# Kernel tuning notes

Measured on AMD Instinct MI355X. Metric: run time of the kernel, lower is better.

Reference implementation:

```python
import jax, jax.numpy as jnp
import numpy as np

B, L, H, E = 2, 2048, 8, 64
S = L  # self-attention


def setup_inputs() -> dict:
    key = jax.random.key(0)
    k1, k2, k3, k4, k5 = jax.random.split(key, 5)
    return {
        "queries": jax.random.normal(k1, (B, L, H, E), dtype=jnp.float32),
        "keys": jax.random.normal(k2, (B, S, H, E), dtype=jnp.float32),
        "values": jax.random.normal(k3, (B, S, H, E), dtype=jnp.float32),
        "tau": jax.random.uniform(k4, (B, 1), dtype=jnp.float32),
        "delta": jax.random.normal(k5, (B, S), dtype=jnp.float32),
    }


def reference(queries, keys, values, tau, delta):
    # De-stationary attention: scores = (QK^T) * tau + delta, causal mask, softmax, AV
    E_ = queries.shape[-1]
    scale = 1.0 / jnp.sqrt(jnp.float32(E_))
    tau_b = tau[:, None, None, :]      # [B,1,1,1]
    delta_b = delta[:, None, None, :]  # [B,1,1,S]
    scores = jnp.einsum('blhe,bshe->bhls', queries, keys) * tau_b + delta_b  # [B,H,L,S]
    Lq, Sk = scores.shape[-2], scores.shape[-1]
    causal = jnp.triu(jnp.ones((Lq, Sk), dtype=bool), k=1)  # True = masked
    scores = jnp.where(causal[None, None], -jnp.inf, scores)
    A = jax.nn.softmax(scale * scores, axis=-1)
    V = jnp.einsum('bhls,bshd->blhd', A, values)
    return V
```

## Files before the change

kernel.cpp:

```cpp
#include <hip/hip_runtime.h>


typedef _Float16 h8 __attribute__((ext_vector_type(8)));
typedef _Float16 h2 __attribute__((ext_vector_type(2)));
typedef float f32x4 __attribute__((ext_vector_type(4)));

constexpr int Bc = 2, Lc = 2048, Hc = 8, Ec = 64, Sc = 2048;
constexpr int QTL = 128;
constexpr int NQT = Lc / QTL;
constexpr int KT = 64;
constexpr int LDK = 72;
constexpr int NBH = Bc * Hc;
constexpr float SCALE = 0.125f;
constexpr float LOG2E = 1.44269504088896340736f;

__device__ __forceinline__ h2 pk2(float x, float y) {
  return __builtin_bit_cast(h2, __builtin_amdgcn_cvt_pkrtz(x, y));
}
template <int CTRL>
__device__ __forceinline__ float dpp_f(float x) {
  int r = __builtin_amdgcn_update_dpp(0, __builtin_bit_cast(int, x), CTRL, 0xF, 0xF, true);
  return __builtin_bit_cast(float, r);
}

template <int CH_IT, int EPB, int NIT>
__global__ __launch_bounds__(256, 2)
void dsattn_fwd(const float* __restrict__ Qg, const float* __restrict__ Kg,
                const float* __restrict__ Vg, const float* __restrict__ taug,
                const float* __restrict__ deltag, float* __restrict__ Og,
                _Float16* __restrict__ Opart, float* __restrict__ Lpart) {
  __shared__ __align__(16) _Float16 Ks[2][KT * LDK];
  __shared__ __align__(16) _Float16 Vt[2][Ec * LDK];
  __shared__ __align__(16) _Float16 Pb[4][16 * LDK];

  const int tid = threadIdx.x;
  const int wave = tid >> 6, lane = tid & 63;
  const int quad = lane >> 4, l16 = lane & 15;
  const int srow = tid >> 2;
  const int sec = (tid & 3) << 4;
  const int vrp = ((tid >> 3) + 4 * (tid & 7)) & 31;
  const int ve8 = (tid & 7) << 3;
  _Float16* pb = &Pb[wave][0];
  const int lo = l16 & 1;
  const int pbase = (lo ? 32 : 0) + (l16 & ~1);

  h8 onesf;
#pragma unroll
  for (int j = 0; j < 8; ++j) onesf[j] = (_Float16)1.0f;

  for (int wid = (int)blockIdx.x; wid < NIT; wid += (int)gridDim.x) {
    const int bh = wid & (NBH - 1);
    const int e = wid >> 4;
    int qt = NQT - 1, c0 = 0, pre_e = 0;
    {
      int ee = e, acc = 0;
#pragma unroll
      for (int q = NQT - 1; q >= 0; --q) {
        const int n = (2 * q + 1 + CH_IT) / CH_IT;
        if (ee < n) { qt = q; c0 = ee; pre_e = EPB - acc - n; break; }
        ee -= n; acc += n;
      }
    }
    const int ntiles = 2 * qt + 2;
    const int nch = (ntiles + CH_IT - 1) / CH_IT;
    const int ktBeg = c0 * CH_IT;
    const int ktEnd = min(ktBeg + CH_IT - 1, ntiles - 1);
    const int q0 = qt * QTL;
    const int b = bh >> 3, h = bh & 7;
    const float ct = taug[b] * (SCALE * LOG2E);

    h8 qfrag[2][2];
#pragma unroll
    for (int f = 0; f < 2; ++f)
#pragma unroll
      for (int kk = 0; kk < 2; ++kk) {
        const float* qp = Qg + (((size_t)b * Lc + q0 + 32 * wave + 16 * f + l16) * Hc + h) * Ec
                         + quad * 8 + kk * 32;
        const float4* p = (const float4*)qp;
        union { h8 v; h2 c[4]; } u;
        float4 a0 = p[0], a1 = p[1];
        u.c[0] = pk2(a0.x, a0.y); u.c[1] = pk2(a0.z, a0.w);
        u.c[2] = pk2(a1.x, a1.y); u.c[3] = pk2(a1.z, a1.w);
        qfrag[f][kk] = u.v;
      }

    f32x4 Oacc[2][4], Osum[2];
#pragma unroll
    for (int f = 0; f < 2; ++f) {
#pragma unroll
      for (int nt = 0; nt < 4; ++nt) Oacc[f][nt] = (f32x4){0.f, 0.f, 0.f, 0.f};
      Osum[f] = (f32x4){0.f, 0.f, 0.f, 0.f};
    }

    float dcur[4];

    __syncthreads();

    {
      const int kb = ktBeg * KT;
      const float* kp = Kg + (((size_t)b * Sc + kb + srow) * Hc + h) * Ec + sec;
      float4 c0v = ((const float4*)kp)[0], c1v = ((const float4*)kp)[1];
      float4 c2v = ((const float4*)kp)[2], c3v = ((const float4*)kp)[3];
      const float* vp0 = Vg + (((size_t)b * Sc + kb + 2 * vrp) * Hc + h) * Ec + ve8;
      const float* vp1 = vp0 + Hc * Ec;
      float4 r00 = ((const float4*)vp0)[0], r01 = ((const float4*)vp0)[1];
      float4 r10 = ((const float4*)vp1)[0], r11 = ((const float4*)vp1)[1];
#pragma unroll
      for (int nt = 0; nt < 4; ++nt)
        dcur[nt] = deltag[(size_t)b * Sc + kb + nt * 16 + l16] * (SCALE * LOG2E);
      union { h8 v; h2 c[4]; } w0, w1;
      w0.c[0] = pk2(c0v.x, c0v.y); w0.c[1] = pk2(c0v.z, c0v.w);
      w0.c[2] = pk2(c1v.x, c1v.y); w0.c[3] = pk2(c1v.z, c1v.w);
      w1.c[0] = pk2(c2v.x, c2v.y); w1.c[1] = pk2(c2v.z, c2v.w);
      w1.c[2] = pk2(c3v.x, c3v.y); w1.c[3] = pk2(c3v.z, c3v.w);
      *(h8*)&Ks[0][srow * LDK + sec] = w0.v;
      *(h8*)&Ks[0][srow * LDK + sec + 8] = w1.v;
      const float e0[8] = {r00.x, r00.y, r00.z, r00.w, r01.x, r01.y, r01.z, r01.w};
      const float e1[8] = {r10.x, r10.y, r10.z, r10.w, r11.x, r11.y, r11.z, r11.w};
#pragma unroll
      for (int j = 0; j < 8; ++j)
        *(h2*)&Vt[0][(ve8 + j) * LDK + 2 * vrp] = pk2(e0[j], e1[j]);
    }

    for (int kt = ktBeg; kt <= ktEnd; ++kt) {
      const int cur = (kt - ktBeg) & 1;
      const bool pf = (kt < ktEnd);
      const int kbase = kt * KT;

      __syncthreads();

      float4 kn0, kn1, kn2, kn3, vn00, vn01, vn10, vn11;
      float dn[4];
      if (pf) {
        const int nb = (kt + 1) * KT;
        const float* kp = Kg + (((size_t)b * Sc + nb + srow) * Hc + h) * Ec + sec;
        kn0 = ((const float4*)kp)[0]; kn1 = ((const float4*)kp)[1];
        kn2 = ((const float4*)kp)[2]; kn3 = ((const float4*)kp)[3];
        const float* vp0 = Vg + (((size_t)b * Sc + nb + 2 * vrp) * Hc + h) * Ec + ve8;
        const float* vp1 = vp0 + Hc * Ec;
        vn00 = ((const float4*)vp0)[0]; vn01 = ((const float4*)vp0)[1];
        vn10 = ((const float4*)vp1)[0]; vn11 = ((const float4*)vp1)[1];
#pragma unroll
        for (int nt = 0; nt < 4; ++nt)
          dn[nt] = deltag[(size_t)b * Sc + nb + nt * 16 + l16];
      }

      const int wtop = q0 + 32 * wave + 31;
      if (kbase <= wtop) {
        f32x4 Sacc[2][4];
#pragma unroll
        for (int f = 0; f < 2; ++f)
#pragma unroll
          for (int nt = 0; nt < 4; ++nt) Sacc[f][nt] = (f32x4){0.f, 0.f, 0.f, 0.f};
#pragma unroll
        for (int kk = 0; kk < 2; ++kk) {
          h8 bf[4];
#pragma unroll
          for (int nt = 0; nt < 4; ++nt)
            bf[nt] = *(const h8*)&Ks[cur][(nt * 16 + l16) * LDK + quad * 8 + kk * 32];
#pragma unroll
          for (int f = 0; f < 2; ++f)
#pragma unroll
            for (int nt = 0; nt < 4; ++nt)
              Sacc[f][nt] = __builtin_amdgcn_mfma_f32_16x16x32_f16(qfrag[f][kk], bf[nt], Sacc[f][nt], 0, 0, 0);
        }

#pragma unroll
        for (int f = 0; f < 2; ++f) {
          const int fr0 = q0 + 32 * wave + 16 * f;
          float sv[4][4];
#pragma unroll
          for (int nt = 0; nt < 4; ++nt)
#pragma unroll
            for (int r = 0; r < 4; ++r)
              sv[nt][r] = Sacc[f][nt][r] * ct + dcur[nt];
          if (kbase + 63 > fr0) {
#pragma unroll
            for (int nt = 0; nt < 4; ++nt) {
              const int key = kbase + nt * 16 + l16;
#pragma unroll
              for (int r = 0; r < 4; ++r)
                if (key > fr0 + quad * 4 + r) sv[nt][r] = -1e30f;
            }
          }
#pragma unroll
          for (int nt = 0; nt < 4; ++nt)
#pragma unroll
            for (int r = 0; r < 4; ++r)
              sv[nt][r] = __builtin_amdgcn_exp2f(sv[nt][r]);

#pragma unroll
          for (int r = 0; r < 4; ++r) {
            float o0 = dpp_f<0xB1>(sv[0][r]);
            float o1 = dpp_f<0xB1>(sv[1][r]);
            float o2 = dpp_f<0xB1>(sv[2][r]);
            float o3 = dpp_f<0xB1>(sv[3][r]);
            h2 d0 = lo ? pk2(o2, sv[2][r]) : pk2(sv[0][r], o0);
            h2 d1 = lo ? pk2(o3, sv[3][r]) : pk2(sv[1][r], o1);
            _Float16* pp = &pb[((quad << 2) + r) * LDK + pbase];
            *(h2*)pp = d0;
            *(h2*)(pp + 16) = d1;
          }
          asm volatile("s_waitcnt lgkmcnt(0)" ::: "memory");

          h8 af0 = *(const h8*)&pb[l16 * LDK + quad * 8];
          h8 af1 = *(const h8*)&pb[l16 * LDK + quad * 8 + 32];

#pragma unroll
          for (int nt = 0; nt < 4; ++nt) {
            h8 vf0 = *(const h8*)&Vt[cur][(nt * 16 + l16) * LDK + quad * 8];
            Oacc[f][nt] = __builtin_amdgcn_mfma_f32_16x16x32_f16(af0, vf0, Oacc[f][nt], 0, 0, 0);
            h8 vf1 = *(const h8*)&Vt[cur][(nt * 16 + l16) * LDK + quad * 8 + 32];
            Oacc[f][nt] = __builtin_amdgcn_mfma_f32_16x16x32_f16(af1, vf1, Oacc[f][nt], 0, 0, 0);
          }
          Osum[f] = __builtin_amdgcn_mfma_f32_16x16x32_f16(af0, onesf, Osum[f], 0, 0, 0);
          Osum[f] = __builtin_amdgcn_mfma_f32_16x16x32_f16(af1, onesf, Osum[f], 0, 0, 0);
        }
      }

      if (pf) {
        _Float16* ksn = &Ks[cur ^ 1][0];
        _Float16* vtn = &Vt[cur ^ 1][0];
        union { h8 v; h2 c[4]; } w0, w1;
        w0.c[0] = pk2(kn0.x, kn0.y); w0.c[1] = pk2(kn0.z, kn0.w);
        w0.c[2] = pk2(kn1.x, kn1.y); w0.c[3] = pk2(kn1.z, kn1.w);
        w1.c[0] = pk2(kn2.x, kn2.y); w1.c[1] = pk2(kn2.z, kn2.w);
        w1.c[2] = pk2(kn3.x, kn3.y); w1.c[3] = pk2(kn3.z, kn3.w);
        *(h8*)&ksn[srow * LDK + sec] = w0.v;
        *(h8*)&ksn[srow * LDK + sec + 8] = w1.v;
        const float e0[8] = {vn00.x, vn00.y, vn00.z, vn00.w, vn01.x, vn01.y, vn01.z, vn01.w};
        const float e1[8] = {vn10.x, vn10.y, vn10.z, vn10.w, vn11.x, vn11.y, vn11.z, vn11.w};
#pragma unroll
        for (int j = 0; j < 8; ++j)
          *(h2*)&vtn[(ve8 + j) * LDK + 2 * vrp] = pk2(e0[j], e1[j]);
#pragma unroll
        for (int nt = 0; nt < 4; ++nt) dcur[nt] = dn[nt] * (SCALE * LOG2E);
      }
    }

    if (nch == 1) {
#pragma unroll
      for (int f = 0; f < 2; ++f)
#pragma unroll
        for (int r = 0; r < 4; ++r) {
          const int qrow = q0 + 32 * wave + 16 * f + (quad << 2) + r;
          const float inv = 1.0f / Osum[f][r];
          float* op = Og + (((size_t)b * Lc + qrow) * Hc + h) * Ec;
#pragma unroll
          for (int nt = 0; nt < 4; ++nt) op[nt * 16 + l16] = Oacc[f][nt][r] * inv;
        }
    } else {
      const int en = bh * EPB + pre_e + c0;
      _Float16* op = Opart + (size_t)en * (QTL * Ec);
#pragma unroll
      for (int f = 0; f < 2; ++f)
#pragma unroll
        for (int r = 0; r < 4; ++r) {
          const int row = 32 * wave + 16 * f + (quad << 2) + r;
#pragma unroll
          for (int nt = 0; nt < 4; ++nt)
            op[row * Ec + nt * 16 + l16] = (_Float16)Oacc[f][nt][r];
          if (l16 == 0) Lpart[en * QTL + row] = Osum[f][r];
        }
    }
  }
}

template <int CH_IT, int EPB>
__global__ __launch_bounds__(256, 4)
void dsattn_comb(const _Float16* __restrict__ Opart, const float* __restrict__ Lpart,
                 float* __restrict__ Og) {
  const int qt = (CH_IT / 2) + ((int)blockIdx.x >> 2);
  const int slab = (int)blockIdx.x & 3;
  const int bh = (int)blockIdx.y;
  const int b = bh >> 3, h = bh & 7;
  const int nch = (2 * qt + 1 + CH_IT) / CH_IT;
  int pre_e = 0;
#pragma unroll
  for (int q = 0; q < NQT; ++q)
    if (q < qt) pre_e += (2 * q + 1 + CH_IT) / CH_IT;
  const int e0 = bh * EPB + pre_e;

  const int row = slab * 32 + ((int)threadIdx.x >> 3);
  const int col = ((int)threadIdx.x & 7) << 3;

  float acc[8];
#pragma unroll
  for (int i = 0; i < 8; ++i) acc[i] = 0.f;
  float l = 0.f;
  for (int c = 0; c < nch; ++c) {
    l += Lpart[(e0 + c) * QTL + row];
    h8 v = *(const h8*)(Opart + (size_t)(e0 + c) * (QTL * Ec) + row * Ec + col);
#pragma unroll
    for (int i = 0; i < 8; ++i) acc[i] += (float)v[i];
  }
  const float inv = 1.0f / l;
  float* out = Og + (((size_t)b * Lc + qt * QTL + row) * Hc + h) * Ec + col;
  float4 o0, o1;
  o0.x = acc[0] * inv; o0.y = acc[1] * inv; o0.z = acc[2] * inv; o0.w = acc[3] * inv;
  o1.x = acc[4] * inv; o1.y = acc[5] * inv; o1.z = acc[6] * inv; o1.w = acc[7] * inv;
  ((float4*)out)[0] = o0;
  ((float4*)out)[1] = o1;
}

extern "C" void kernel_launch(void* const* d_in, const int* in_sizes, int n_in,
                              void* d_out, int out_size, void* d_ws, size_t ws_size,
                              hipStream_t stream) {
  const float* Q = (const float*)d_in[0];
  const float* K = (const float*)d_in[1];
  const float* V = (const float*)d_in[2];
  const float* tau = (const float*)d_in[3];
  const float* delta = (const float*)d_in[4];
  float* O = (float*)d_out;

  constexpr int CH = 4;
  constexpr int EPB = 72;
  constexpr int TOT_E = Bc * Hc * EPB;
  constexpr int PERS = 768;
  const size_t need = (size_t)TOT_E * QTL * Ec * 2 + (size_t)TOT_E * QTL * 4;

  if (ws_size >= need) {
    _Float16* Opart = (_Float16*)d_ws;
    float* Lpart = (float*)(Opart + (size_t)TOT_E * QTL * Ec);
    dsattn_fwd<CH, EPB, TOT_E><<<dim3(PERS), 256, 0, stream>>>(
        Q, K, V, tau, delta, O, Opart, Lpart);
    dim3 g2((NQT - CH / 2) * 4, Bc * Hc);
    dsattn_comb<CH, EPB><<<g2, 256, 0, stream>>>(Opart, Lpart, O);
  } else {
    dsattn_fwd<32, NQT, NQT * NBH><<<dim3(NQT * NBH), 256, 0, stream>>>(
        Q, K, V, tau, delta, O, nullptr, nullptr);
  }
}
```

Measured before the change: 109.9 us.

## Pre-convert K/V to swizzled fp16 and stream tiles with global_load_lds

```diff
diff --git a/kernel.cpp b/kernel.cpp
--- a/kernel.cpp
+++ b/kernel.cpp
@@ -9,10 +9,48 @@
 constexpr int QTL = 128;
 constexpr int NQT = Lc / QTL;
 constexpr int KT = 64;
-constexpr int LDK = 72;
 constexpr int NBH = Bc * Hc;
+constexpr int CH = 4;
+constexpr int EPB = 72;
+constexpr int NIT = NBH * EPB;
 constexpr float SCALE = 0.125f;
 constexpr float LOG2E = 1.44269504088896340736f;
+
+__constant__ int d_qtbase[16] = {0,1,2,4,6,9,12,16,20,25,30,36,42,49,56,64};
+__constant__ signed char d_eqt[72] = {
+  15,15,15,15,15,15,15,15,
+  14,14,14,14,14,14,14,
+  13,13,13,13,13,13,13,
+  12,12,12,12,12,12,
+  11,11,11,11,11,11,
+  10,10,10,10,10,
+   9, 9, 9, 9, 9,
+   8, 8, 8, 8,
+   7, 7, 7, 7,
+   6, 6, 6,
+   5, 5, 5,
+   4, 4,
+   3, 3,
+   2,
+   1,
+  14,12,10, 8, 6, 4, 2, 0};
+__constant__ signed char d_ec0[72] = {
+   0, 1, 2, 3, 4, 5, 6, 7,
+   0, 1, 2, 3, 4, 5, 6,
+   0, 1, 2, 3, 4, 5, 6,
+   0, 1, 2, 3, 4, 5,
+   0, 1, 2, 3, 4, 5,
+   0, 1, 2, 3, 4,
+   0, 1, 2, 3, 4,
+   0, 1, 2, 3,
+   0, 1, 2, 3,
+   0, 1, 2,
+   0, 1, 2,
+   0, 1,
+   0, 1,
+   0,
+   0,
+   7, 6, 5, 4, 3, 2, 1, 0};
 
 __device__ __forceinline__ h2 pk2(float x, float y) {
   return __builtin_bit_cast(h2, __builtin_amdgcn_cvt_pkrtz(x, y));
@@ -22,18 +60,321 @@
   int r = __builtin_amdgcn_update_dpp(0, __builtin_bit_cast(int, x), CTRL, 0xF, 0xF, true);
   return __builtin_bit_cast(float, r);
 }
-
-template <int CH_IT, int EPB, int NIT>
+__device__ __forceinline__ void gl16(const void* g, void* l) {
+  __builtin_amdgcn_global_load_lds(
+      (const __attribute__((address_space(1))) void*)g,
+      (__attribute__((address_space(3))) void*)l, 16, 0, 0);
+}
+
+__global__ __launch_bounds__(256, 4)
+void dsattn_prep(const float* __restrict__ Kg, const float* __restrict__ Vg,
+                 _Float16* __restrict__ Kh, _Float16* __restrict__ Vh) {
+  __shared__ __align__(16) _Float16 T[64][72];
+  const int kt = (int)blockIdx.x;
+  const int bh = (int)blockIdx.y;
+  const int b = bh >> 3, h = bh & 7;
+  const int tid = (int)threadIdx.x;
+  const int sr = tid >> 2;
+  const int e0 = (tid & 3) << 4;
+  const int s = kt * KT + sr;
+
+  {
+    const float* kp = Kg + (((size_t)b * Sc + s) * Hc + h) * Ec + e0;
+    float4 a0 = ((const float4*)kp)[0], a1 = ((const float4*)kp)[1];
+    float4 a2 = ((const float4*)kp)[2], a3 = ((const float4*)kp)[3];
+    union { h8 v; h2 c[4]; } u0, u1;
+    u0.c[0] = pk2(a0.x, a0.y); u0.c[1] = pk2(a0.z, a0.w);
+    u0.c[2] = pk2(a1.x, a1.y); u0.c[3] = pk2(a1.z, a1.w);
+    u1.c[0] = pk2(a2.x, a2.y); u1.c[1] = pk2(a2.z, a2.w);
+    u1.c[2] = pk2(a3.x, a3.y); u1.c[3] = pk2(a3.z, a3.w);
+    char* out = (char*)Kh + (((size_t)bh * Sc + s) << 7);
+    const int sl = e0 >> 3;
+    const int rx = (sr & 7) << 4;
+    *(h8*)(out + ((sl << 4) ^ rx)) = u0.v;
+    *(h8*)(out + (((sl + 1) << 4) ^ rx)) = u1.v;
+  }
+
+  {
+    const float* vp = Vg + (((size_t)b * Sc + s) * Hc + h) * Ec + e0;
+    float4 v0 = ((const float4*)vp)[0], v1 = ((const float4*)vp)[1];
+    float4 v2 = ((const float4*)vp)[2], v3 = ((const float4*)vp)[3];
+    const float ev[16] = {v0.x, v0.y, v0.z, v0.w, v1.x, v1.y, v1.z, v1.w,
+                          v2.x, v2.y, v2.z, v2.w, v3.x, v3.y, v3.z, v3.w};
+#pragma unroll
+    for (int j = 0; j < 8; ++j) {
+      h2 t = pk2(ev[2 * j], ev[2 * j + 1]);
+      T[e0 + 2 * j][sr] = t[0];
+      T[e0 + 2 * j + 1][sr] = t[1];
+    }
+  }
+  __syncthreads();
+  {
+    const int er = tid >> 2;
+    const int k0 = (tid & 3) << 4;
+    h8 w0 = *(const h8*)&T[er][k0];
+    h8 w1 = *(const h8*)&T[er][k0 + 8];
+    char* out = (char*)Vh + (((size_t)bh * 32 + kt) << 13) + er * 128;
+    const int sl = k0 >> 3;
+    const int rx = (er & 7) << 4;
+    *(h8*)(out + ((sl << 4) ^ rx)) = w0;
+    *(h8*)(out + (((sl + 1) << 4) ^ rx)) = w1;
+  }
+}
+
+__global__ __launch_bounds__(256, 4)
+void dsattn_fwd_main(const float* __restrict__ Qg, const _Float16* __restrict__ Kh,
+                     const _Float16* __restrict__ Vh, const float* __restrict__ taug,
+                     const float* __restrict__ deltag, float* __restrict__ Og,
+                     _Float16* __restrict__ Opart, float* __restrict__ Lpart) {
+  __shared__ __align__(16) _Float16 Ks[2][KT * 64];
+  __shared__ __align__(16) _Float16 Vt[2][Ec * 64];
+  __shared__ __align__(16) _Float16 Pb[4][16 * 64];
+
+  const int tid = (int)threadIdx.x;
+  const int wave = tid >> 6, lane = tid & 63;
+  const int quad = lane >> 4, l16 = lane & 15;
+  _Float16* pb = &Pb[wave][0];
+  const int lo = l16 & 1;
+  const int pbase = (lo ? 32 : 0) + (l16 & ~1);
+  const int kx = (l16 & 7) << 3;
+  const int koff0 = (quad * 8) ^ kx;
+  const int koff1 = (quad * 8 + 32) ^ kx;
+
+  h8 onesf;
+#pragma unroll
+  for (int j = 0; j < 8; ++j) onesf[j] = (_Float16)1.0f;
+
+  for (int it = (int)blockIdx.x; it < NIT; it += (int)gridDim.x) {
+    const int xcd = it & 7;
+    const int r_ = it >> 3;
+    const int bh = (xcd << 1) | (r_ & 1);
+    const int e = r_ >> 1;
+    const int qt = d_eqt[e], c0 = d_ec0[e];
+    const int ntiles = 2 * qt + 2;
+    const int nch = (ntiles + CH - 1) / CH;
+    const int ktBeg = c0 * CH;
+    const int ktEnd = min(ktBeg + CH - 1, ntiles - 1);
+    const int q0 = qt * QTL;
+    const int b = bh >> 3, h = bh & 7;
+    const float ct = taug[b] * (SCALE * LOG2E);
+
+    h8 qfrag[2][2];
+#pragma unroll
+    for (int f = 0; f < 2; ++f)
+#pragma unroll
+      for (int kk = 0; kk < 2; ++kk) {
+        const float* qp = Qg + (((size_t)b * Lc + q0 + 32 * wave + 16 * f + l16) * Hc + h) * Ec
+                         + quad * 8 + kk * 32;
+        const float4* p = (const float4*)qp;
+        union { h8 v; h2 c[4]; } u;
+        float4 a0 = p[0], a1 = p[1];
+        u.c[0] = pk2(a0.x, a0.y); u.c[1] = pk2(a0.z, a0.w);
+        u.c[2] = pk2(a1.x, a1.y); u.c[3] = pk2(a1.z, a1.w);
+        qfrag[f][kk] = u.v;
+      }
+
+    f32x4 Oacc[2][4], Osum[2];
+#pragma unroll
+    for (int f = 0; f < 2; ++f) {
+#pragma unroll
+      for (int nt = 0; nt < 4; ++nt) Oacc[f][nt] = (f32x4){0.f, 0.f, 0.f, 0.f};
+      Osum[f] = (f32x4){0.f, 0.f, 0.f, 0.f};
+    }
+    float dcur[4];
+
+    __syncthreads();
+
+    {
+      const char* kg = (const char*)Kh + (((size_t)bh * Sc + (size_t)ktBeg * KT) << 7)
+                       + wave * 2048 + lane * 16;
+      const char* vg = (const char*)Vh + (((size_t)bh * 32 + ktBeg) << 13)
+                       + wave * 2048 + lane * 16;
+      char* kl = (char*)&Ks[0][0] + wave * 2048;
+      char* vl = (char*)&Vt[0][0] + wave * 2048;
+      gl16(kg, kl); gl16(kg + 1024, kl + 1024);
+      gl16(vg, vl); gl16(vg + 1024, vl + 1024);
+#pragma unroll
+      for (int nt = 0; nt < 4; ++nt)
+        dcur[nt] = deltag[(size_t)b * Sc + ktBeg * KT + nt * 16 + l16] * (SCALE * LOG2E);
+    }
+
+    for (int kt = ktBeg; kt <= ktEnd; ++kt) {
+      const int cur = (kt - ktBeg) & 1;
+      const bool pf = (kt < ktEnd);
+      const int kbase = kt * KT;
+
+      __syncthreads();
+
+      float dn[4];
+      if (pf) {
+        const char* kg = (const char*)Kh + (((size_t)bh * Sc + (size_t)(kt + 1) * KT) << 7)
+                         + wave * 2048 + lane * 16;
+        const char* vg = (const char*)Vh + (((size_t)bh * 32 + kt + 1) << 13)
+                         + wave * 2048 + lane * 16;
+        char* kl = (char*)&Ks[cur ^ 1][0] + wave * 2048;
+        char* vl = (char*)&Vt[cur ^ 1][0] + wave * 2048;
+        gl16(kg, kl); gl16(kg + 1024, kl + 1024);
+        gl16(vg, vl); gl16(vg + 1024, vl + 1024);
+#pragma unroll
+        for (int nt = 0; nt < 4; ++nt)
+          dn[nt] = deltag[(size_t)b * Sc + (kt + 1) * KT + nt * 16 + l16];
+      }
+
+      const int wtop = q0 + 32 * wave + 31;
+      if (kbase <= wtop) {
+        f32x4 Sacc[2][4];
+#pragma unroll
+        for (int f = 0; f < 2; ++f)
+#pragma unroll
+          for (int nt = 0; nt < 4; ++nt) Sacc[f][nt] = (f32x4){0.f, 0.f, 0.f, 0.f};
+        __builtin_amdgcn_s_setprio(1);
+#pragma unroll
+        for (int kk = 0; kk < 2; ++kk) {
+          const int ko = kk ? koff1 : koff0;
+          h8 bf[4];
+#pragma unroll
+          for (int nt = 0; nt < 4; ++nt)
+            bf[nt] = *(const h8*)&Ks[cur][(nt * 16 + l16) * 64 + ko];
+#pragma unroll
+          for (int f = 0; f < 2; ++f)
+#pragma unroll
+            for (int nt = 0; nt < 4; ++nt)
+              Sacc[f][nt] = __builtin_amdgcn_mfma_f32_16x16x32_f16(qfrag[f][kk], bf[nt], Sacc[f][nt], 0, 0, 0);
+        }
+        __builtin_amdgcn_s_setprio(0);
+
+#pragma unroll
+        for (int f = 0; f < 2; ++f) {
+          const int fr0 = q0 + 32 * wave + 16 * f;
+          float sv[4][4];
+#pragma unroll
+          for (int nt = 0; nt < 4; ++nt)
+#pragma unroll
+            for (int rr = 0; rr < 4; ++rr)
+              sv[nt][rr] = Sacc[f][nt][rr] * ct + dcur[nt];
+          if (kbase + 63 > fr0) {
+#pragma unroll
+            for (int nt = 0; nt < 4; ++nt) {
+              const int key = kbase + nt * 16 + l16;
+#pragma unroll
+              for (int rr = 0; rr < 4; ++rr)
+                if (key > fr0 + quad * 4 + rr) sv[nt][rr] = -1e30f;
+            }
+          }
+#pragma unroll
+          for (int nt = 0; nt < 4; ++nt)
+#pragma unroll
+            for (int rr = 0; rr < 4; ++rr)
+              sv[nt][rr] = __builtin_amdgcn_exp2f(sv[nt][rr]);
+
+#pragma unroll
+          for (int rr = 0; rr < 4; ++rr) {
+            float o0 = dpp_f<0xB1>(sv[0][rr]);
+            float o1 = dpp_f<0xB1>(sv[1][rr]);
+            float o2 = dpp_f<0xB1>(sv[2][rr]);
+            float o3 = dpp_f<0xB1>(sv[3][rr]);
+            h2 d0 = lo ? pk2(o2, sv[2][rr]) : pk2(sv[0][rr], o0);
+            h2 d1 = lo ? pk2(o3, sv[3][rr]) : pk2(sv[1][rr], o1);
+            const int row = (quad << 2) + rr;
+            char* pr = (char*)pb + row * 128;
+            const int rx = (row & 7) << 4;
+            *(h2*)(pr + ((pbase * 2) ^ rx)) = d0;
+            *(h2*)(pr + ((pbase * 2 + 32) ^ rx)) = d1;
+          }
+          asm volatile("s_waitcnt lgkmcnt(0)" ::: "memory");
+
+          h8 af0 = *(const h8*)&pb[l16 * 64 + koff0];
+          h8 af1 = *(const h8*)&pb[l16 * 64 + koff1];
+
+          __builtin_amdgcn_s_setprio(1);
+#pragma unroll
+          for (int nt = 0; nt < 4; ++nt) {
+            h8 vf0 = *(const h8*)&Vt[cur][(nt * 16 + l16) * 64 + koff0];
+            Oacc[f][nt] = __builtin_amdgcn_mfma_f32_16x16x32_f16(af0, vf0, Oacc[f][nt], 0, 0, 0);
+            h8 vf1 = *(const h8*)&Vt[cur][(nt * 16 + l16) * 64 + koff1];
+            Oacc[f][nt] = __builtin_amdgcn_mfma_f32_16x16x32_f16(af1, vf1, Oacc[f][nt], 0, 0, 0);
+          }
+          Osum[f] = __builtin_amdgcn_mfma_f32_16x16x32_f16(af0, onesf, Osum[f], 0, 0, 0);
+          Osum[f] = __builtin_amdgcn_mfma_f32_16x16x32_f16(af1, onesf, Osum[f], 0, 0, 0);
+          __builtin_amdgcn_s_setprio(0);
+        }
+      }
+
+      if (pf) {
+#pragma unroll
+        for (int nt = 0; nt < 4; ++nt) dcur[nt] = dn[nt] * (SCALE * LOG2E);
+      }
+    }
+
+    if (nch == 1) {
+#pragma unroll
+      for (int f = 0; f < 2; ++f)
+#pragma unroll
+        for (int rr = 0; rr < 4; ++rr) {
+          const int qrow = q0 + 32 * wave + 16 * f + (quad << 2) + rr;
+          const float inv = 1.0f / Osum[f][rr];
+          float* op = Og + (((size_t)b * Lc + qrow) * Hc + h) * Ec;
+#pragma unroll
+          for (int nt = 0; nt < 4; ++nt) op[nt * 16 + l16] = Oacc[f][nt][rr] * inv;
+        }
+    } else {
+      const int en = bh * EPB + d_qtbase[qt] + c0;
+      _Float16* op = Opart + (size_t)en * (QTL * Ec);
+#pragma unroll
+      for (int f = 0; f < 2; ++f)
+#pragma unroll
+        for (int rr = 0; rr < 4; ++rr) {
+          const int row = 32 * wave + 16 * f + (quad << 2) + rr;
+#pragma unroll
+          for (int nt = 0; nt < 4; ++nt)
+            op[row * Ec + nt * 16 + l16] = (_Float16)Oacc[f][nt][rr];
+          if (l16 == 0) Lpart[en * QTL + row] = Osum[f][rr];
+        }
+    }
+  }
+}
+
+__global__ __launch_bounds__(256, 4)
+void dsattn_comb_main(const _Float16* __restrict__ Opart, const float* __restrict__ Lpart,
+                      float* __restrict__ Og) {
+  const int qt = 2 + ((int)blockIdx.x >> 2);
+  const int slab = (int)blockIdx.x & 3;
+  const int bh = (int)blockIdx.y;
+  const int b = bh >> 3, h = bh & 7;
+  const int nch = (2 * qt + 1 + CH) / CH;
+  const int e0 = bh * EPB + d_qtbase[qt];
+  const int row = slab * 32 + ((int)threadIdx.x >> 3);
+  const int col = ((int)threadIdx.x & 7) << 3;
+
+  float acc[8];
+#pragma unroll
+  for (int i = 0; i < 8; ++i) acc[i] = 0.f;
+  float l = 0.f;
+  for (int c = 0; c < nch; ++c) {
+    l += Lpart[(e0 + c) * QTL + row];
+    h8 v = *(const h8*)(Opart + (size_t)(e0 + c) * (QTL * Ec) + row * Ec + col);
+#pragma unroll
+    for (int i = 0; i < 8; ++i) acc[i] += (float)v[i];
+  }
+  const float inv = 1.0f / l;
+  float* out = Og + (((size_t)b * Lc + qt * QTL + row) * Hc + h) * Ec + col;
+  float4 o0, o1;
+  o0.x = acc[0] * inv; o0.y = acc[1] * inv; o0.z = acc[2] * inv; o0.w = acc[3] * inv;
+  o1.x = acc[4] * inv; o1.y = acc[5] * inv; o1.z = acc[6] * inv; o1.w = acc[7] * inv;
+  ((float4*)out)[0] = o0;
+  ((float4*)out)[1] = o1;
+}
+
 __global__ __launch_bounds__(256, 2)
-void dsattn_fwd(const float* __restrict__ Qg, const float* __restrict__ Kg,
-                const float* __restrict__ Vg, const float* __restrict__ taug,
-                const float* __restrict__ deltag, float* __restrict__ Og,
-                _Float16* __restrict__ Opart, float* __restrict__ Lpart) {
+void dsattn_fwd_mono(const float* __restrict__ Qg, const float* __restrict__ Kg,
+                     const float* __restrict__ Vg, const float* __restrict__ taug,
+                     const float* __restrict__ deltag, float* __restrict__ Og) {
+  constexpr int LDK = 72;
   __shared__ __align__(16) _Float16 Ks[2][KT * LDK];
   __shared__ __align__(16) _Float16 Vt[2][Ec * LDK];
   __shared__ __align__(16) _Float16 Pb[4][16 * LDK];
 
-  const int tid = threadIdx.x;
+  const int tid = (int)threadIdx.x;
   const int wave = tid >> 6, lane = tid & 63;
   const int quad = lane >> 4, l16 = lane & 15;
   const int srow = tid >> 2;
@@ -48,23 +389,10 @@
 #pragma unroll
   for (int j = 0; j < 8; ++j) onesf[j] = (_Float16)1.0f;
 
-  for (int wid = (int)blockIdx.x; wid < NIT; wid += (int)gridDim.x) {
+  for (int wid = (int)blockIdx.x; wid < NQT * NBH; wid += (int)gridDim.x) {
     const int bh = wid & (NBH - 1);
-    const int e = wid >> 4;
-    int qt = NQT - 1, c0 = 0, pre_e = 0;
-    {
-      int ee = e, acc = 0;
-#pragma unroll
-      for (int q = NQT - 1; q >= 0; --q) {
-        const int n = (2 * q + 1 + CH_IT) / CH_IT;
-        if (ee < n) { qt = q; c0 = ee; pre_e = EPB - acc - n; break; }
-        ee -= n; acc += n;
-      }
-    }
-    const int ntiles = 2 * qt + 2;
-    const int nch = (ntiles + CH_IT - 1) / CH_IT;
-    const int ktBeg = c0 * CH_IT;
-    const int ktEnd = min(ktBeg + CH_IT - 1, ntiles - 1);
+    const int qt = NQT - 1 - (wid >> 4);
+    const int ktEnd = 2 * qt + 1;
     const int q0 = qt * QTL;
     const int b = bh >> 3, h = bh & 7;
     const float ct = taug[b] * (SCALE * LOG2E);
@@ -91,23 +419,21 @@
       for (int nt = 0; nt < 4; ++nt) Oacc[f][nt] = (f32x4){0.f, 0.f, 0.f, 0.f};
       Osum[f] = (f32x4){0.f, 0.f, 0.f, 0.f};
     }
-
     float dcur[4];
 
     __syncthreads();
 
     {
-      const int kb = ktBeg * KT;
-      const float* kp = Kg + (((size_t)b * Sc + kb + srow) * Hc + h) * Ec + sec;
+      const float* kp = Kg + (((size_t)b * Sc + srow) * Hc + h) * Ec + sec;
       float4 c0v = ((const float4*)kp)[0], c1v = ((const float4*)kp)[1];
       float4 c2v = ((const float4*)kp)[2], c3v = ((const float4*)kp)[3];
-      const float* vp0 = Vg + (((size_t)b * Sc + kb + 2 * vrp) * Hc + h) * Ec + ve8;
+      const float* vp0 = Vg + (((size_t)b * Sc + 2 * vrp) * Hc + h) * Ec + ve8;
       const float* vp1 = vp0 + Hc * Ec;
       float4 r00 = ((const float4*)vp0)[0], r01 = ((const float4*)vp0)[1];
       float4 r10 = ((const float4*)vp1)[0], r11 = ((const float4*)vp1)[1];
 #pragma unroll
       for (int nt = 0; nt < 4; ++nt)
-        dcur[nt] = deltag[(size_t)b * Sc + kb + nt * 16 + l16] * (SCALE * LOG2E);
+        dcur[nt] = deltag[(size_t)b * Sc + nt * 16 + l16] * (SCALE * LOG2E);
       union { h8 v; h2 c[4]; } w0, w1;
       w0.c[0] = pk2(c0v.x, c0v.y); w0.c[1] = pk2(c0v.z, c0v.w);
       w0.c[2] = pk2(c1v.x, c1v.y); w0.c[3] = pk2(c1v.z, c1v.w);
@@ -122,8 +448,8 @@
         *(h2*)&Vt[0][(ve8 + j) * LDK + 2 * vrp] = pk2(e0[j], e1[j]);
     }
 
-    for (int kt = ktBeg; kt <= ktEnd; ++kt) {
-      const int cur = (kt - ktBeg) & 1;
+    for (int kt = 0; kt <= ktEnd; ++kt) {
+      const int cur = kt & 1;
       const bool pf = (kt < ktEnd);
       const int kbase = kt * KT;
 
@@ -172,32 +498,32 @@
 #pragma unroll
           for (int nt = 0; nt < 4; ++nt)
 #pragma unroll
-            for (int r = 0; r < 4; ++r)
-              sv[nt][r] = Sacc[f][nt][r] * ct + dcur[nt];
+            for (int rr = 0; rr < 4; ++rr)
+              sv[nt][rr] = Sacc[f][nt][rr] * ct + dcur[nt];
           if (kbase + 63 > fr0) {
 #pragma unroll
             for (int nt = 0; nt < 4; ++nt) {
               const int key = kbase + nt * 16 + l16;
 #pragma unroll
-              for (int r = 0; r < 4; ++r)
-                if (key > fr0 + quad * 4 + r) sv[nt][r] = -1e30f;
+              for (int rr = 0; rr < 4; ++rr)
+                if (key > fr0 + quad * 4 + rr) sv[nt][rr] = -1e30f;
             }
           }
 #pragma unroll
           for (int nt = 0; nt < 4; ++nt)
 #pragma unroll
-            for (int r = 0; r < 4; ++r)
-              sv[nt][r] = __builtin_amdgcn_exp2f(sv[nt][r]);
-
-#pragma unroll
-          for (int r = 0; r < 4; ++r) {
-            float o0 = dpp_f<0xB1>(sv[0][r]);
-            float o1 = dpp_f<0xB1>(sv[1][r]);
-            float o2 = dpp_f<0xB1>(sv[2][r]);
-            float o3 = dpp_f<0xB1>(sv[3][r]);
-            h2 d0 = lo ? pk2(o2, sv[2][r]) : pk2(sv[0][r], o0);
-            h2 d1 = lo ? pk2(o3, sv[3][r]) : pk2(sv[1][r], o1);
-            _Float16* pp = &pb[((quad << 2) + r) * LDK + pbase];
+            for (int rr = 0; rr < 4; ++rr)
+              sv[nt][rr] = __builtin_amdgcn_exp2f(sv[nt][rr]);
+
+#pragma unroll
+          for (int rr = 0; rr < 4; ++rr) {
+            float o0 = dpp_f<0xB1>(sv[0][rr]);
+            float o1 = dpp_f<0xB1>(sv[1][rr]);
+            float o2 = dpp_f<0xB1>(sv[2][rr]);
+            float o3 = dpp_f<0xB1>(sv[3][rr]);
+            h2 d0 = lo ? pk2(o2, sv[2][rr]) : pk2(sv[0][rr], o0);
+            h2 d1 = lo ? pk2(o3, sv[3][rr]) : pk2(sv[1][rr], o1);
+            _Float16* pp = &pb[((quad << 2) + rr) * LDK + pbase];
             *(h2*)pp = d0;
             *(h2*)(pp + 16) = d1;
           }
@@ -238,69 +564,17 @@
       }
     }
 
-    if (nch == 1) {
-#pragma unroll
-      for (int f = 0; f < 2; ++f)
-#pragma unroll
-        for (int r = 0; r < 4; ++r) {
-          const int qrow = q0 + 32 * wave + 16 * f + (quad << 2) + r;
-          const float inv = 1.0f / Osum[f][r];
-          float* op = Og + (((size_t)b * Lc + qrow) * Hc + h) * Ec;
-#pragma unroll
-          for (int nt = 0; nt < 4; ++nt) op[nt * 16 + l16] = Oacc[f][nt][r] * inv;
-        }
-    } else {
-      const int en = bh * EPB + pre_e + c0;
-      _Float16* op = Opart + (size_t)en * (QTL * Ec);
-#pragma unroll
-      for (int f = 0; f < 2; ++f)
-#pragma unroll
-        for (int r = 0; r < 4; ++r) {
-          const int row = 32 * wave + 16 * f + (quad << 2) + r;
-#pragma unroll
-          for (int nt = 0; nt < 4; ++nt)
-            op[row * Ec + nt * 16 + l16] = (_Float16)Oacc[f][nt][r];
-          if (l16 == 0) Lpart[en * QTL + row] = Osum[f][r];
-        }
-    }
+#pragma unroll
+    for (int f = 0; f < 2; ++f)
+#pragma unroll
+      for (int rr = 0; rr < 4; ++rr) {
+        const int qrow = q0 + 32 * wave + 16 * f + (quad << 2) + rr;
+        const float inv = 1.0f / Osum[f][rr];
+        float* op = Og + (((size_t)b * Lc + qrow) * Hc + h) * Ec;
+#pragma unroll
+        for (int nt = 0; nt < 4; ++nt) op[nt * 16 + l16] = Oacc[f][nt][rr] * inv;
+      }
   }
-}
-
-template <int CH_IT, int EPB>
-__global__ __launch_bounds__(256, 4)
-void dsattn_comb(const _Float16* __restrict__ Opart, const float* __restrict__ Lpart,
-                 float* __restrict__ Og) {
-  const int qt = (CH_IT / 2) + ((int)blockIdx.x >> 2);
-  const int slab = (int)blockIdx.x & 3;
-  const int bh = (int)blockIdx.y;
-  const int b = bh >> 3, h = bh & 7;
-  const int nch = (2 * qt + 1 + CH_IT) / CH_IT;
-  int pre_e = 0;
-#pragma unroll
-  for (int q = 0; q < NQT; ++q)
-    if (q < qt) pre_e += (2 * q + 1 + CH_IT) / CH_IT;
-  const int e0 = bh * EPB + pre_e;
-
-  const int row = slab * 32 + ((int)threadIdx.x >> 3);
-  const int col = ((int)threadIdx.x & 7) << 3;
-
-  float acc[8];
-#pragma unroll
-  for (int i = 0; i < 8; ++i) acc[i] = 0.f;
-  float l = 0.f;
-  for (int c = 0; c < nch; ++c) {
-    l += Lpart[(e0 + c) * QTL + row];
-    h8 v = *(const h8*)(Opart + (size_t)(e0 + c) * (QTL * Ec) + row * Ec + col);
-#pragma unroll
-    for (int i = 0; i < 8; ++i) acc[i] += (float)v[i];
-  }
-  const float inv = 1.0f / l;
-  float* out = Og + (((size_t)b * Lc + qt * QTL + row) * Hc + h) * Ec + col;
-  float4 o0, o1;
-  o0.x = acc[0] * inv; o0.y = acc[1] * inv; o0.z = acc[2] * inv; o0.w = acc[3] * inv;
-  o1.x = acc[4] * inv; o1.y = acc[5] * inv; o1.z = acc[6] * inv; o1.w = acc[7] * inv;
-  ((float4*)out)[0] = o0;
-  ((float4*)out)[1] = o1;
 }
 
 extern "C" void kernel_launch(void* const* d_in, const int* in_sizes, int n_in,
@@ -313,21 +587,21 @@
   const float* delta = (const float*)d_in[4];
   float* O = (float*)d_out;
 
-  constexpr int CH = 4;
-  constexpr int EPB = 72;
-  constexpr int TOT_E = Bc * Hc * EPB;
-  constexpr int PERS = 768;
-  const size_t need = (size_t)TOT_E * QTL * Ec * 2 + (size_t)TOT_E * QTL * 4;
+  const size_t needOp = (size_t)NIT * QTL * Ec * 2;
+  const size_t needLp = (size_t)NIT * QTL * 4;
+  const size_t needKh = (size_t)NBH * Sc * Ec * 2;
+  const size_t needVh = needKh;
+  const size_t need = needOp + needLp + needKh + needVh;
 
   if (ws_size >= need) {
     _Float16* Opart = (_Float16*)d_ws;
-    float* Lpart = (float*)(Opart + (size_t)TOT_E * QTL * Ec);
-    dsattn_fwd<CH, EPB, TOT_E><<<dim3(PERS), 256, 0, stream>>>(
-        Q, K, V, tau, delta, O, Opart, Lpart);
-    dim3 g2((NQT - CH / 2) * 4, Bc * Hc);
-    dsattn_comb<CH, EPB><<<g2, 256, 0, stream>>>(Opart, Lpart, O);
+    float* Lpart = (float*)((char*)d_ws + needOp);
+    _Float16* Kh = (_Float16*)((char*)d_ws + needOp + needLp);
+    _Float16* Vh = (_Float16*)((char*)d_ws + needOp + needLp + needKh);
+    dsattn_prep<<<dim3(Sc / KT, NBH), 256, 0, stream>>>(K, V, Kh, Vh);
+    dsattn_fwd_main<<<dim3(NIT), 256, 0, stream>>>(Q, Kh, Vh, tau, delta, O, Opart, Lpart);
+    dsattn_comb_main<<<dim3((NQT - CH / 2) * 4, NBH), 256, 0, stream>>>(Opart, Lpart, O);
   } else {
-    dsattn_fwd<32, NQT, NQT * NBH><<<dim3(NQT * NBH), 256, 0, stream>>>(
-        Q, K, V, tau, delta, O, nullptr, nullptr);
+    dsattn_fwd_mono<<<dim3(NQT * NBH), 256, 0, stream>>>(Q, K, V, tau, delta, O);
   }
 }
```

After: 147.8 us. 1.34x slower.
